# Kernel optimization log

Hardware: AMD Instinct MI355X
Metric: run time of the kernel (lower is better)

## Reference

```python
import jax, jax.numpy as jnp
import numpy as np
from jax import lax

VOCAB = 50257
EMB = 512
HID = 1024
SEQ = 4096
NUM_LAYERS = 2


def _lstm_layer(x_seq, h0, c0, w_ih, w_hh, b_ih, b_hh):
    """Single-layer LSTM over time. x_seq: [T, in], h0/c0: [H].
    PyTorch gate order: i, f, g, o."""
    # Precompute input projections for all timesteps: [T, 4H]
    xg = x_seq @ w_ih.T + (b_ih + b_hh)

    def step(carry, xg_t):
        h, c = carry
        g = xg_t + h @ w_hh.T  # [4H]
        i, f, gg, o = jnp.split(g, 4)
        i = jax.nn.sigmoid(i)
        f = jax.nn.sigmoid(f)
        gg = jnp.tanh(gg)
        o = jax.nn.sigmoid(o)
        c_new = f * c + i * gg
        h_new = o * jnp.tanh(c_new)
        return (h_new, c_new), h_new

    (h_n, c_n), hs = lax.scan(step, (h0, c0), xg)
    return hs, h_n, c_n  # hs: [T, H]


def setup_inputs() -> dict:
    key = jax.random.key(0)
    ks = jax.random.split(key, 12)
    s = 0.02
    inp = {
        "input": jax.random.randint(ks[0], (SEQ,), 0, VOCAB),
        "h0": jnp.zeros((NUM_LAYERS, 1, HID), jnp.float32),
        "c0": jnp.zeros((NUM_LAYERS, 1, HID), jnp.float32),
        "emb": jax.random.normal(ks[1], (VOCAB, EMB), jnp.float32) * s,
        "w_ih0": jax.random.normal(ks[2], (4 * HID, EMB), jnp.float32) * s,
        "w_hh0": jax.random.normal(ks[3], (4 * HID, HID), jnp.float32) * s,
        "b_ih0": jnp.zeros((4 * HID,), jnp.float32),
        "b_hh0": jnp.zeros((4 * HID,), jnp.float32),
        "w_ih1": jax.random.normal(ks[4], (4 * HID, HID), jnp.float32) * s,
        "w_hh1": jax.random.normal(ks[5], (4 * HID, HID), jnp.float32) * s,
        "b_ih1": jnp.zeros((4 * HID,), jnp.float32),
        "b_hh1": jnp.zeros((4 * HID,), jnp.float32),
        "w_out": jax.random.normal(ks[6], (VOCAB, HID), jnp.float32) * s,
        "b_out": jnp.zeros((VOCAB,), jnp.float32),
    }
    return inp


def reference(input, h0, c0, emb, w_ih0, w_hh0, b_ih0, b_hh0,
              w_ih1, w_hh1, b_ih1, b_hh1, w_out, b_out):
    # Embedding gather: [T, EMB] (batch dim of 1 is implicit)
    x = emb[input]
    # Layer 0
    hs0, h_n0, c_n0 = _lstm_layer(x, h0[0, 0], c0[0, 0], w_ih0, w_hh0, b_ih0, b_hh0)
    # Layer 1 consumes layer-0 hidden sequence
    hs1, h_n1, c_n1 = _lstm_layer(hs0, h0[1, 0], c0[1, 0], w_ih1, w_hh1, b_ih1, b_hh1)
    # lstm_out[-1]: [1, H]
    last = hs1[-1][None, :]
    logits = last @ w_out.T + b_out  # [1, VOCAB]
    output = jax.nn.log_softmax(logits, axis=1)
    h_n = jnp.stack([h_n0, h_n1])[:, None, :]  # [2, 1, H]
    c_n = jnp.stack([c_n0, c_n1])[:, None, :]
    return output, h_n, c_n
```

## Files before the change

### kernel.cpp

```cpp
#include <hip/hip_runtime.h>


#define T_SEQ 4096
#define HID   1024
#define EMBD  512
#define VOCAB 50257
#define NBLK  256
#define TPB   256
#define UB    4

#define WS_H0T 0
#define WS_H1T 2048
#define WS_H1F 4096
#define WS_LOG 5120
#define WS_LSE 55377

#define OFF_W0 0
#define OFF_W1 49152
#define OFF_V0 114688
#define OFF_V1 120832
#define OFF_PP 124928
#define OFF_FL 125056
#define SMEM_BYTES 125088

#define FL_SF0 0
#define FL_SF1 1
#define FL_PA1 2
#define FL_C3  3

typedef __attribute__((ext_vector_type(8))) short short8;
typedef __attribute__((ext_vector_type(4))) float f32x4;
typedef unsigned long long u64;

__device__ __forceinline__ unsigned short f2bf(float f) {
  unsigned int u = __float_as_uint(f);
  u += 0x7FFFu + ((u >> 16) & 1u);
  return (unsigned short)(u >> 16);
}
__device__ __forceinline__ unsigned int pack2bf(float a, float b) {
  return (unsigned int)f2bf(a) | ((unsigned int)f2bf(b) << 16);
}
__device__ __forceinline__ float sigmoidf_(float x) {
  return 1.f / (1.f + __expf(-x));
}
__device__ __forceinline__ float tanhf_(float x) {
  return 1.f - 2.f / (__expf(2.f * x) + 1.f);
}
__device__ __forceinline__ unsigned ldsacq(const unsigned* p) {
  return __hip_atomic_load(p, __ATOMIC_ACQUIRE, __HIP_MEMORY_SCOPE_WORKGROUP);
}
__device__ __forceinline__ void ldsrel(unsigned* p, unsigned v) {
  __hip_atomic_store(p, v, __ATOMIC_RELEASE, __HIP_MEMORY_SCOPE_WORKGROUP);
}
__device__ __forceinline__ u64 agld(const u64* p) {
  return __hip_atomic_load(p, __ATOMIC_RELAXED, __HIP_MEMORY_SCOPE_AGENT);
}
__device__ __forceinline__ void agst(u64* p, u64 v) {
  __hip_atomic_store(p, v, __ATOMIC_RELAXED, __HIP_MEMORY_SCOPE_AGENT);
}

template<int NS>
__device__ __forceinline__ f32x4 mm_lds(const short8* vf, const short8* wf,
                                        int grp, int lane) {
  f32x4 a0 = {0.f, 0.f, 0.f, 0.f};
  f32x4 a1 = a0, a2 = a0, a3 = a0;
#pragma unroll
  for (int i = 0; i < NS; ++i) {
    short8 av = vf[i * 4 + grp];
    short8 bv = wf[i * 64 + lane];
    if ((i & 3) == 0)      a0 = __builtin_amdgcn_mfma_f32_16x16x32_bf16(av, bv, a0, 0, 0, 0);
    else if ((i & 3) == 1) a1 = __builtin_amdgcn_mfma_f32_16x16x32_bf16(av, bv, a1, 0, 0, 0);
    else if ((i & 3) == 2) a2 = __builtin_amdgcn_mfma_f32_16x16x32_bf16(av, bv, a2, 0, 0, 0);
    else                   a3 = __builtin_amdgcn_mfma_f32_16x16x32_bf16(av, bv, a3, 0, 0, 0);
  }
  return (a0 + a1) + (a2 + a3);
}

__global__ __launch_bounds__(512, 1) void reset_kernel(
    const float* __restrict__ h0in, unsigned int* __restrict__ ws) {
  const int tid = threadIdx.x;
  u64* H0T = reinterpret_cast<u64*>(ws + WS_H0T);
  u64* H1T = reinterpret_cast<u64*>(ws + WS_H1T);
  agst(&H0T[tid], (u64)pack2bf(h0in[2 * tid], h0in[2 * tid + 1]));
  agst(&H1T[tid], (u64)pack2bf(h0in[HID + 2 * tid], h0in[HID + 2 * tid + 1]));
  agst(&H0T[512 + tid], 0xFFFFFFFF00000000ULL);
  agst(&H1T[512 + tid], 0xFFFFFFFF00000000ULL);
}

__global__ __launch_bounds__(TPB, 1) void scan_kernel(
    const int* __restrict__ tok,
    const float* __restrict__ h0in, const float* __restrict__ c0in,
    const float* __restrict__ emb,
    const float* __restrict__ wih0, const float* __restrict__ whh0,
    const float* __restrict__ bih0, const float* __restrict__ bhh0,
    const float* __restrict__ wih1, const float* __restrict__ whh1,
    const float* __restrict__ bih1, const float* __restrict__ bhh1,
    float* __restrict__ dout, unsigned int* __restrict__ ws) {
  extern __shared__ char smem[];
  short8* W0f = reinterpret_cast<short8*>(smem + OFF_W0);
  short8* W1f = reinterpret_cast<short8*>(smem + OFF_W1);
  unsigned int* v0w = reinterpret_cast<unsigned int*>(smem + OFF_V0);
  unsigned int* v1w = reinterpret_cast<unsigned int*>(smem + OFF_V1);
  const short8* v0f = reinterpret_cast<const short8*>(smem + OFF_V0);
  const short8* v1f = reinterpret_cast<const short8*>(smem + OFF_V1);
  float* pp  = reinterpret_cast<float*>(smem + OFF_PP);
  unsigned* flg = reinterpret_cast<unsigned*>(smem + OFF_FL);

  const int tid = threadIdx.x;
  const int bid = blockIdx.x;
  const int lane = tid & 63;
  const int w = tid >> 6;
  const int grp = lane >> 4;

  for (int slot = tid; slot < 48 * 64; slot += TPB) {
    const int seg = slot >> 6, l = slot & 63;
    const int col = l & 15, g = l >> 4;
    const int grow = (col >> 2) * HID + bid * UB + (col & 3);
    const int k0 = seg * 32 + g * 8;
    const float* src = (k0 < EMBD) ? (wih0 + (size_t)grow * EMBD + k0)
                                   : (whh0 + (size_t)grow * HID + (k0 - EMBD));
    const float4* s4 = reinterpret_cast<const float4*>(src);
    float4 f0 = s4[0], f1 = s4[1];
    short8 pk;
    pk[0] = (short)f2bf(f0.x); pk[1] = (short)f2bf(f0.y);
    pk[2] = (short)f2bf(f0.z); pk[3] = (short)f2bf(f0.w);
    pk[4] = (short)f2bf(f1.x); pk[5] = (short)f2bf(f1.y);
    pk[6] = (short)f2bf(f1.z); pk[7] = (short)f2bf(f1.w);
    W0f[slot] = pk;
  }
  for (int slot = tid; slot < 64 * 64; slot += TPB) {
    const int seg = slot >> 6, l = slot & 63;
    const int col = l & 15, g = l >> 4;
    const int grow = (col >> 2) * HID + bid * UB + (col & 3);
    const int k0 = seg * 32 + g * 8;
    const float* src = (k0 < HID) ? (wih1 + (size_t)grow * HID + k0)
                                  : (whh1 + (size_t)grow * HID + (k0 - HID));
    const float4* s4 = reinterpret_cast<const float4*>(src);
    float4 f0 = s4[0], f1 = s4[1];
    short8 pk;
    pk[0] = (short)f2bf(f0.x); pk[1] = (short)f2bf(f0.y);
    pk[2] = (short)f2bf(f0.z); pk[3] = (short)f2bf(f0.w);
    pk[4] = (short)f2bf(f1.x); pk[5] = (short)f2bf(f1.y);
    pk[6] = (short)f2bf(f1.z); pk[7] = (short)f2bf(f1.w);
    W1f[slot] = pk;
  }
  if (tid < 8) flg[tid] = 1u;

  u64* H0T = reinterpret_cast<u64*>(ws + WS_H0T);
  u64* H1T = reinterpret_cast<u64*>(ws + WS_H1T);

  __syncthreads();

  if (w == 0) {
    float bs0 = 0.f;
    if (lane < 16) {
      const int grow = (lane >> 2) * HID + bid * UB + (lane & 3);
      bs0 = bih0[grow] + bhh0[grow];
    }
    float cst = (lane < UB) ? c0in[bid * UB + lane] : 0.f;

    const float4* e4 = reinterpret_cast<const float4*>(emb) + (size_t)tok[0] * 128;
    float4 xA = e4[lane], xB = e4[64 + lane];

    for (int r = 1; r <= T_SEQ + 1; ++r) {
      const int p = r & 1;
      if (r >= 3) {
        const unsigned need = (unsigned)(r - 2);
        while (ldsacq(&flg[FL_PA1]) < need) { }
      }
      if (r <= T_SEQ) {
        u64* vx = reinterpret_cast<u64*>(v0w + p * 768);
        vx[lane]      = (u64)pack2bf(xA.x, xA.y) | ((u64)pack2bf(xA.z, xA.w) << 32);
        vx[64 + lane] = (u64)pack2bf(xB.x, xB.y) | ((u64)pack2bf(xB.z, xB.w) << 32);
        if (r <= T_SEQ - 1) {
          const float4* en = reinterpret_cast<const float4*>(emb) + (size_t)tok[r] * 128;
          xA = en[lane]; xB = en[64 + lane];
        }
      }
      {
        const unsigned tg = (unsigned)(r - 1);
        const u64* ap = &H0T[((r - 1) & 1) * 512 + lane];
        u64 d0, d1, d2, d3, d4, d5, d6, d7;
        for (;;) {
          d0 = agld(ap);        d1 = agld(ap + 64);  d2 = agld(ap + 128);
          d3 = agld(ap + 192);  d4 = agld(ap + 256); d5 = agld(ap + 320);
          d6 = agld(ap + 384);  d7 = agld(ap + 448);
          if ((unsigned)(d0 >> 32) == tg && (unsigned)(d1 >> 32) == tg &&
              (unsigned)(d2 >> 32) == tg && (unsigned)(d3 >> 32) == tg &&
              (unsigned)(d4 >> 32) == tg && (unsigned)(d5 >> 32) == tg &&
              (unsigned)(d6 >> 32) == tg && (unsigned)(d7 >> 32) == tg) break;
        }
        unsigned* dst = v0w + p * 768 + 256 + lane;
        dst[0] = (unsigned)d0;   dst[64] = (unsigned)d1;
        dst[128] = (unsigned)d2; dst[192] = (unsigned)d3;
        dst[256] = (unsigned)d4; dst[320] = (unsigned)d5;
        dst[384] = (unsigned)d6; dst[448] = (unsigned)d7;
      }
      ldsrel(&flg[FL_SF0], (unsigned)r);

      if (r <= T_SEQ) {
        f32x4 s = mm_lds<48>(v0f + p * 192, W0f, grp, lane);
        float g = (lane < 16) ? (s[0] + bs0) : 0.f;
        const int u = lane & 3;
        const float gi = __shfl(g, u),      gf = __shfl(g, 4 + u);
        const float gg = __shfl(g, 8 + u),  go = __shfl(g, 12 + u);
        float hv = 0.f;
        if (lane < UB) {
          const float c = sigmoidf_(gf) * cst + sigmoidf_(gi) * tanhf_(gg);
          cst = c;
          hv = sigmoidf_(go) * tanhf_(c);
          if (r == T_SEQ) {
            dout[VOCAB + bid * UB + lane] = hv;
            dout[VOCAB + 2 * HID + bid * UB + lane] = c;
          }
        }
        const float a = __shfl(hv, 2 * (lane & 1));
        const float b = __shfl(hv, 2 * (lane & 1) + 1);
        if (lane < 2)
          agst(&H0T[(r & 1) * 512 + bid * 2 + lane],
               ((u64)(unsigned)r << 32) | (u64)pack2bf(a, b));
      }
    }
  } else if (w == 1) {
    for (int r = 2; r <= T_SEQ + 1; ++r) {
      const int p = r & 1;
      if (r >= 4) {
        const unsigned need = (unsigned)(r - 2);
        while (ldsacq(&flg[FL_C3]) < need) { }
      }
      const unsigned tg = (unsigned)(r - 2);
      const u64* ap = &H1T[p * 512 + lane];
      u64 d0, d1, d2, d3, d4, d5, d6, d7;
      for (;;) {
        d0 = agld(ap);        d1 = agld(ap + 64);  d2 = agld(ap + 128);
        d3 = agld(ap + 192);  d4 = agld(ap + 256); d5 = agld(ap + 320);
        d6 = agld(ap + 384);  d7 = agld(ap + 448);
        if ((unsigned)(d0 >> 32) == tg && (unsigned)(d1 >> 32) == tg &&
            (unsigned)(d2 >> 32) == tg && (unsigned)(d3 >> 32) == tg &&
            (unsigned)(d4 >> 32) == tg && (unsigned)(d5 >> 32) == tg &&
            (unsigned)(d6 >> 32) == tg && (unsigned)(d7 >> 32) == tg) break;
      }
      unsigned* dst = v1w + p * 512 + lane;
      dst[0] = (unsigned)d0;   dst[64] = (unsigned)d1;
      dst[128] = (unsigned)d2; dst[192] = (unsigned)d3;
      dst[256] = (unsigned)d4; dst[320] = (unsigned)d5;
      dst[384] = (unsigned)d6; dst[448] = (unsigned)d7;
      ldsrel(&flg[FL_SF1], (unsigned)r);
    }
  } else if (w == 2) {
    for (int r = 2; r <= T_SEQ + 1; ++r) {
      const int p = r & 1;
      const unsigned ru = (unsigned)r;
      while (ldsacq(&flg[FL_SF0]) < ru) { }
      f32x4 s = mm_lds<32>(v0f + p * 192 + 64, W1f, grp, lane);
      if (lane < 16) pp[p * 16 + lane] = s[0];
      ldsrel(&flg[FL_PA1], ru);
    }
  } else {
    float bs1 = 0.f;
    if (lane < 16) {
      const int grow = (lane >> 2) * HID + bid * UB + (lane & 3);
      bs1 = bih1[grow] + bhh1[grow];
    }
    float cst = (lane < UB) ? c0in[HID + bid * UB + lane] : 0.f;
    for (int r = 2; r <= T_SEQ + 1; ++r) {
      const int p = r & 1;
      const unsigned ru = (unsigned)r;
      while (ldsacq(&flg[FL_SF1]) < ru) { }
      f32x4 s = mm_lds<32>(v1f + p * 128, W1f + 32 * 64, grp, lane);
      ldsrel(&flg[FL_C3], ru);
      while (ldsacq(&flg[FL_PA1]) < ru) { }
      float g = (lane < 16) ? (s[0] + pp[p * 16 + lane] + bs1) : 0.f;
      const int u = lane & 3;
      const float gi = __shfl(g, u),      gf = __shfl(g, 4 + u);
      const float gg = __shfl(g, 8 + u),  go = __shfl(g, 12 + u);
      float hv = 0.f;
      if (lane < UB) {
        const float c = sigmoidf_(gf) * cst + sigmoidf_(gi) * tanhf_(gg);
        cst = c;
        hv = sigmoidf_(go) * tanhf_(c);
        if (r == T_SEQ + 1) {
          float* h1f = reinterpret_cast<float*>(ws + WS_H1F);
          h1f[bid * UB + lane] = hv;
          dout[VOCAB + HID + bid * UB + lane] = hv;
          dout[VOCAB + 3 * HID + bid * UB + lane] = c;
        }
      }
      const float a = __shfl(hv, 2 * (lane & 1));
      const float b = __shfl(hv, 2 * (lane & 1) + 1);
      if (lane < 2)
        agst(&H1T[((r - 1) & 1) * 512 + bid * 2 + lane],
             ((u64)(unsigned)(r - 1) << 32) | (u64)pack2bf(a, b));
    }
  }
}

__global__ __launch_bounds__(256) void logits_kernel(
    const float* __restrict__ wout, const float* __restrict__ bout,
    unsigned int* __restrict__ ws) {
  const float* h1f = reinterpret_cast<const float*>(ws + WS_H1F);
  float* lg = reinterpret_cast<float*>(ws + WS_LOG);
  const int lane = threadIdx.x & 63;
  const int wv = threadIdx.x >> 6;
  const int gw = blockIdx.x * 4 + wv;
  const float4* h4 = reinterpret_cast<const float4*>(h1f);
  float4 h[4];
#pragma unroll
  for (int j = 0; j < 4; ++j) h[j] = h4[j * 64 + lane];
  for (int v = gw; v < VOCAB; v += 1024) {
    const float4* wr = reinterpret_cast<const float4*>(wout + (size_t)v * HID);
    float s = 0.f;
#pragma unroll
    for (int j = 0; j < 4; ++j) {
      float4 x = wr[j * 64 + lane];
      s += x.x * h[j].x + x.y * h[j].y + x.z * h[j].z + x.w * h[j].w;
    }
#pragma unroll
    for (int m = 32; m >= 1; m >>= 1) s += __shfl_xor(s, m, 64);
    if (lane == 0) lg[v] = s + bout[v];
  }
}

__global__ __launch_bounds__(1024) void lse_kernel(unsigned int* __restrict__ ws) {
  const float* lg = reinterpret_cast<const float*>(ws + WS_LOG);
  __shared__ float wred[16];
  __shared__ float mshare;
  const int tid = threadIdx.x;
  float m = -3.4e38f;
  for (int i = tid; i < VOCAB; i += 1024) m = fmaxf(m, lg[i]);
#pragma unroll
  for (int s = 32; s >= 1; s >>= 1) m = fmaxf(m, __shfl_xor(m, s, 64));
  if ((tid & 63) == 0) wred[tid >> 6] = m;
  __syncthreads();
  if (tid == 0) {
    float mm = wred[0];
    for (int i = 1; i < 16; ++i) mm = fmaxf(mm, wred[i]);
    mshare = mm;
  }
  __syncthreads();
  const float M = mshare;
  float a = 0.f;
  for (int i = tid; i < VOCAB; i += 1024) a += __expf(lg[i] - M);
#pragma unroll
  for (int s = 32; s >= 1; s >>= 1) a += __shfl_xor(a, s, 64);
  __syncthreads();
  if ((tid & 63) == 0) wred[tid >> 6] = a;
  __syncthreads();
  if (tid == 0) {
    float ss = 0.f;
    for (int i = 0; i < 16; ++i) ss += wred[i];
    reinterpret_cast<float*>(ws + WS_LSE)[0] = M + logf(ss);
  }
}

__global__ __launch_bounds__(256) void out_kernel(
    const unsigned int* __restrict__ ws, float* __restrict__ dout) {
  const float lse = reinterpret_cast<const float*>(ws + WS_LSE)[0];
  const float* lg = reinterpret_cast<const float*>(ws + WS_LOG);
  const int i = blockIdx.x * 256 + threadIdx.x;
  if (i < VOCAB) dout[i] = lg[i] - lse;
}

extern "C" void kernel_launch(void* const* d_in, const int* in_sizes, int n_in,
                              void* d_out, int out_size, void* d_ws, size_t ws_size,
                              hipStream_t stream) {
  const int*   tok  = (const int*)d_in[0];
  const float* h0in = (const float*)d_in[1];
  const float* c0in = (const float*)d_in[2];
  const float* emb  = (const float*)d_in[3];
  const float* wih0 = (const float*)d_in[4];
  const float* whh0 = (const float*)d_in[5];
  const float* bih0 = (const float*)d_in[6];
  const float* bhh0 = (const float*)d_in[7];
  const float* wih1 = (const float*)d_in[8];
  const float* whh1 = (const float*)d_in[9];
  const float* bih1 = (const float*)d_in[10];
  const float* bhh1 = (const float*)d_in[11];
  const float* wout = (const float*)d_in[12];
  const float* bout = (const float*)d_in[13];
  float* out = (float*)d_out;
  unsigned int* ws = (unsigned int*)d_ws;

  (void)in_sizes; (void)n_in; (void)out_size; (void)ws_size;

  (void)hipFuncSetAttribute((const void*)scan_kernel,
                            hipFuncAttributeMaxDynamicSharedMemorySize, SMEM_BYTES);

  reset_kernel<<<1, 512, 0, stream>>>(h0in, ws);
  scan_kernel<<<NBLK, TPB, SMEM_BYTES, stream>>>(
      tok, h0in, c0in, emb, wih0, whh0, bih0, bhh0,
      wih1, whh1, bih1, bhh1, out, ws);
  logits_kernel<<<256, 256, 0, stream>>>(wout, bout, ws);
  lse_kernel<<<1, 1024, 0, stream>>>(ws);
  out_kernel<<<(VOCAB + 255) / 256, 256, 0, stream>>>(ws, out);
}
```

Before: 13.36 ms.

## Mirror hidden-state exchange buffers across eight copies and poll only unready words

```diff
diff --git a/kernel.cpp b/kernel.cpp
--- a/kernel.cpp
+++ b/kernel.cpp
@@ -8,12 +8,13 @@
 #define NBLK  256
 #define TPB   256
 #define UB    4
+#define NMIR  8
 
 #define WS_H0T 0
-#define WS_H1T 2048
-#define WS_H1F 4096
-#define WS_LOG 5120
-#define WS_LSE 55377
+#define WS_H1T 16384
+#define WS_H1F 32768
+#define WS_LOG 33792
+#define WS_LSE 84049
 
 #define OFF_W0 0
 #define OFF_W1 49152
@@ -81,10 +82,15 @@
   const int tid = threadIdx.x;
   u64* H0T = reinterpret_cast<u64*>(ws + WS_H0T);
   u64* H1T = reinterpret_cast<u64*>(ws + WS_H1T);
-  agst(&H0T[tid], (u64)pack2bf(h0in[2 * tid], h0in[2 * tid + 1]));
-  agst(&H1T[tid], (u64)pack2bf(h0in[HID + 2 * tid], h0in[HID + 2 * tid + 1]));
-  agst(&H0T[512 + tid], 0xFFFFFFFF00000000ULL);
-  agst(&H1T[512 + tid], 0xFFFFFFFF00000000ULL);
+  const u64 w0 = (u64)pack2bf(h0in[2 * tid], h0in[2 * tid + 1]);
+  const u64 w1 = (u64)pack2bf(h0in[HID + 2 * tid], h0in[HID + 2 * tid + 1]);
+#pragma unroll
+  for (int m = 0; m < NMIR; ++m) {
+    agst(&H0T[m * 1024 + tid], w0);
+    agst(&H0T[m * 1024 + 512 + tid], 0xFFFFFFFF00000000ULL);
+    agst(&H1T[m * 1024 + tid], w1);
+    agst(&H1T[m * 1024 + 512 + tid], 0xFFFFFFFF00000000ULL);
+  }
 }
 
 __global__ __launch_bounds__(TPB, 1) void scan_kernel(
@@ -111,6 +117,7 @@
   const int lane = tid & 63;
   const int w = tid >> 6;
   const int grp = lane >> 4;
+  const int mymir = bid & 7;
 
   for (int slot = tid; slot < 48 * 64; slot += TPB) {
     const int seg = slot >> 6, l = slot & 63;
@@ -179,16 +186,20 @@
       }
       {
         const unsigned tg = (unsigned)(r - 1);
-        const u64* ap = &H0T[((r - 1) & 1) * 512 + lane];
-        u64 d0, d1, d2, d3, d4, d5, d6, d7;
+        const u64* ap = &H0T[mymir * 1024 + ((r - 1) & 1) * 512 + lane];
+        u64 d0 = 0, d1 = 0, d2 = 0, d3 = 0, d4 = 0, d5 = 0, d6 = 0, d7 = 0;
+        bool k0 = false, k1 = false, k2 = false, k3 = false;
+        bool k4 = false, k5 = false, k6 = false, k7 = false;
         for (;;) {
-          d0 = agld(ap);        d1 = agld(ap + 64);  d2 = agld(ap + 128);
-          d3 = agld(ap + 192);  d4 = agld(ap + 256); d5 = agld(ap + 320);
-          d6 = agld(ap + 384);  d7 = agld(ap + 448);
-          if ((unsigned)(d0 >> 32) == tg && (unsigned)(d1 >> 32) == tg &&
-              (unsigned)(d2 >> 32) == tg && (unsigned)(d3 >> 32) == tg &&
-              (unsigned)(d4 >> 32) == tg && (unsigned)(d5 >> 32) == tg &&
-              (unsigned)(d6 >> 32) == tg && (unsigned)(d7 >> 32) == tg) break;
+          if (!k0) { d0 = agld(ap);       k0 = ((unsigned)(d0 >> 32) == tg); }
+          if (!k1) { d1 = agld(ap + 64);  k1 = ((unsigned)(d1 >> 32) == tg); }
+          if (!k2) { d2 = agld(ap + 128); k2 = ((unsigned)(d2 >> 32) == tg); }
+          if (!k3) { d3 = agld(ap + 192); k3 = ((unsigned)(d3 >> 32) == tg); }
+          if (!k4) { d4 = agld(ap + 256); k4 = ((unsigned)(d4 >> 32) == tg); }
+          if (!k5) { d5 = agld(ap + 320); k5 = ((unsigned)(d5 >> 32) == tg); }
+          if (!k6) { d6 = agld(ap + 384); k6 = ((unsigned)(d6 >> 32) == tg); }
+          if (!k7) { d7 = agld(ap + 448); k7 = ((unsigned)(d7 >> 32) == tg); }
+          if (k0 && k1 && k2 && k3 && k4 && k5 && k6 && k7) break;
         }
         unsigned* dst = v0w + p * 768 + 256 + lane;
         dst[0] = (unsigned)d0;   dst[64] = (unsigned)d1;
@@ -216,8 +227,8 @@
         }
         const float a = __shfl(hv, 2 * (lane & 1));
         const float b = __shfl(hv, 2 * (lane & 1) + 1);
-        if (lane < 2)
-          agst(&H0T[(r & 1) * 512 + bid * 2 + lane],
+        if (lane < 16)
+          agst(&H0T[(lane >> 1) * 1024 + (r & 1) * 512 + bid * 2 + (lane & 1)],
                ((u64)(unsigned)r << 32) | (u64)pack2bf(a, b));
       }
     }
@@ -229,16 +240,20 @@
         while (ldsacq(&flg[FL_C3]) < need) { }
       }
       const unsigned tg = (unsigned)(r - 2);
-      const u64* ap = &H1T[p * 512 + lane];
-      u64 d0, d1, d2, d3, d4, d5, d6, d7;
+      const u64* ap = &H1T[mymir * 1024 + p * 512 + lane];
+      u64 d0 = 0, d1 = 0, d2 = 0, d3 = 0, d4 = 0, d5 = 0, d6 = 0, d7 = 0;
+      bool k0 = false, k1 = false, k2 = false, k3 = false;
+      bool k4 = false, k5 = false, k6 = false, k7 = false;
       for (;;) {
-        d0 = agld(ap);        d1 = agld(ap + 64);  d2 = agld(ap + 128);
-        d3 = agld(ap + 192);  d4 = agld(ap + 256); d5 = agld(ap + 320);
-        d6 = agld(ap + 384);  d7 = agld(ap + 448);
-        if ((unsigned)(d0 >> 32) == tg && (unsigned)(d1 >> 32) == tg &&
-            (unsigned)(d2 >> 32) == tg && (unsigned)(d3 >> 32) == tg &&
-            (unsigned)(d4 >> 32) == tg && (unsigned)(d5 >> 32) == tg &&
-            (unsigned)(d6 >> 32) == tg && (unsigned)(d7 >> 32) == tg) break;
+        if (!k0) { d0 = agld(ap);       k0 = ((unsigned)(d0 >> 32) == tg); }
+        if (!k1) { d1 = agld(ap + 64);  k1 = ((unsigned)(d1 >> 32) == tg); }
+        if (!k2) { d2 = agld(ap + 128); k2 = ((unsigned)(d2 >> 32) == tg); }
+        if (!k3) { d3 = agld(ap + 192); k3 = ((unsigned)(d3 >> 32) == tg); }
+        if (!k4) { d4 = agld(ap + 256); k4 = ((unsigned)(d4 >> 32) == tg); }
+        if (!k5) { d5 = agld(ap + 320); k5 = ((unsigned)(d5 >> 32) == tg); }
+        if (!k6) { d6 = agld(ap + 384); k6 = ((unsigned)(d6 >> 32) == tg); }
+        if (!k7) { d7 = agld(ap + 448); k7 = ((unsigned)(d7 >> 32) == tg); }
+        if (k0 && k1 && k2 && k3 && k4 && k5 && k6 && k7) break;
       }
       unsigned* dst = v1w + p * 512 + lane;
       dst[0] = (unsigned)d0;   dst[64] = (unsigned)d1;
@@ -288,8 +303,8 @@
       }
       const float a = __shfl(hv, 2 * (lane & 1));
       const float b = __shfl(hv, 2 * (lane & 1) + 1);
-      if (lane < 2)
-        agst(&H1T[((r - 1) & 1) * 512 + bid * 2 + lane],
+      if (lane < 16)
+        agst(&H1T[(lane >> 1) * 1024 + ((r - 1) & 1) * 512 + bid * 2 + (lane & 1)],
              ((u64)(unsigned)(r - 1) << 32) | (u64)pack2bf(a, b));
     }
   }
```

Measured after the change: 17.19 ms. +28.7%, slower.

## Split layer-0 recurrent gather across two waves and overlap input MFMAs with polling

Applied to the files above, without the earlier changes.

```diff
diff --git a/kernel.cpp b/kernel.cpp
--- a/kernel.cpp
+++ b/kernel.cpp
@@ -23,10 +23,11 @@
 #define OFF_FL 125056
 #define SMEM_BYTES 125088
 
-#define FL_SF0 0
-#define FL_SF1 1
-#define FL_PA1 2
-#define FL_C3  3
+#define FL_SF0A 0
+#define FL_SF0B 1
+#define FL_SF1  2
+#define FL_PA1  3
+#define FL_C3   4
 
 typedef __attribute__((ext_vector_type(8))) short short8;
 typedef __attribute__((ext_vector_type(4))) float f32x4;
@@ -60,20 +61,14 @@
 }
 
 template<int NS>
-__device__ __forceinline__ f32x4 mm_lds(const short8* vf, const short8* wf,
-                                        int grp, int lane) {
-  f32x4 a0 = {0.f, 0.f, 0.f, 0.f};
-  f32x4 a1 = a0, a2 = a0, a3 = a0;
+__device__ __forceinline__ void mm_acc(f32x4 (&acc)[4], const short8* vf,
+                                       const short8* wf, int grp, int lane) {
 #pragma unroll
   for (int i = 0; i < NS; ++i) {
     short8 av = vf[i * 4 + grp];
     short8 bv = wf[i * 64 + lane];
-    if ((i & 3) == 0)      a0 = __builtin_amdgcn_mfma_f32_16x16x32_bf16(av, bv, a0, 0, 0, 0);
-    else if ((i & 3) == 1) a1 = __builtin_amdgcn_mfma_f32_16x16x32_bf16(av, bv, a1, 0, 0, 0);
-    else if ((i & 3) == 2) a2 = __builtin_amdgcn_mfma_f32_16x16x32_bf16(av, bv, a2, 0, 0, 0);
-    else                   a3 = __builtin_amdgcn_mfma_f32_16x16x32_bf16(av, bv, a3, 0, 0, 0);
-  }
-  return (a0 + a1) + (a2 + a3);
+    acc[i & 3] = __builtin_amdgcn_mfma_f32_16x16x32_bf16(av, bv, acc[i & 3], 0, 0, 0);
+  }
 }
 
 __global__ __launch_bounds__(512, 1) void reset_kernel(
@@ -164,42 +159,52 @@
 
     for (int r = 1; r <= T_SEQ + 1; ++r) {
       const int p = r & 1;
-      if (r >= 3) {
-        const unsigned need = (unsigned)(r - 2);
-        while (ldsacq(&flg[FL_PA1]) < need) { }
-      }
+      f32x4 acc[4];
+      acc[0] = f32x4{0.f, 0.f, 0.f, 0.f};
+      acc[1] = acc[0]; acc[2] = acc[0]; acc[3] = acc[0];
+
       if (r <= T_SEQ) {
         u64* vx = reinterpret_cast<u64*>(v0w + p * 768);
         vx[lane]      = (u64)pack2bf(xA.x, xA.y) | ((u64)pack2bf(xA.z, xA.w) << 32);
         vx[64 + lane] = (u64)pack2bf(xB.x, xB.y) | ((u64)pack2bf(xB.z, xB.w) << 32);
+        mm_acc<16>(acc, v0f + p * 192, W0f, grp, lane);
         if (r <= T_SEQ - 1) {
           const float4* en = reinterpret_cast<const float4*>(emb) + (size_t)tok[r] * 128;
           xA = en[lane]; xB = en[64 + lane];
         }
       }
+
+      if (r >= 3) {
+        const unsigned need = (unsigned)(r - 2);
+        while (ldsacq(&flg[FL_PA1]) < need) { }
+      }
       {
         const unsigned tg = (unsigned)(r - 1);
         const u64* ap = &H0T[((r - 1) & 1) * 512 + lane];
-        u64 d0, d1, d2, d3, d4, d5, d6, d7;
+        u64 d0 = 0, d1 = 0, d2 = 0, d3 = 0;
+        bool k0 = false, k1 = false, k2 = false, k3 = false;
         for (;;) {
-          d0 = agld(ap);        d1 = agld(ap + 64);  d2 = agld(ap + 128);
-          d3 = agld(ap + 192);  d4 = agld(ap + 256); d5 = agld(ap + 320);
-          d6 = agld(ap + 384);  d7 = agld(ap + 448);
-          if ((unsigned)(d0 >> 32) == tg && (unsigned)(d1 >> 32) == tg &&
-              (unsigned)(d2 >> 32) == tg && (unsigned)(d3 >> 32) == tg &&
-              (unsigned)(d4 >> 32) == tg && (unsigned)(d5 >> 32) == tg &&
-              (unsigned)(d6 >> 32) == tg && (unsigned)(d7 >> 32) == tg) break;
+          if (!k0) { d0 = agld(ap);       k0 = ((unsigned)(d0 >> 32) == tg); }
+          if (!k1) { d1 = agld(ap + 64);  k1 = ((unsigned)(d1 >> 32) == tg); }
+          if (!k2) { d2 = agld(ap + 128); k2 = ((unsigned)(d2 >> 32) == tg); }
+          if (!k3) { d3 = agld(ap + 192); k3 = ((unsigned)(d3 >> 32) == tg); }
+          if (k0 && k1 && k2 && k3) break;
         }
         unsigned* dst = v0w + p * 768 + 256 + lane;
         dst[0] = (unsigned)d0;   dst[64] = (unsigned)d1;
         dst[128] = (unsigned)d2; dst[192] = (unsigned)d3;
-        dst[256] = (unsigned)d4; dst[320] = (unsigned)d5;
-        dst[384] = (unsigned)d6; dst[448] = (unsigned)d7;
-      }
-      ldsrel(&flg[FL_SF0], (unsigned)r);
+      }
+      ldsrel(&flg[FL_SF0A], (unsigned)r);
 
       if (r <= T_SEQ) {
-        f32x4 s = mm_lds<48>(v0f + p * 192, W0f, grp, lane);
+        mm_acc<16>(acc, v0f + p * 192 + 64, W0f + 16 * 64, grp, lane);
+        {
+          const unsigned ru = (unsigned)r;
+          while (ldsacq(&flg[FL_SF0B]) < ru) { }
+        }
+        mm_acc<16>(acc, v0f + p * 192 + 128, W0f + 32 * 64, grp, lane);
+
+        f32x4 s = (acc[0] + acc[1]) + (acc[2] + acc[3]);
         float g = (lane < 16) ? (s[0] + bs0) : 0.f;
         const int u = lane & 3;
         const float gi = __shfl(g, u),      gf = __shfl(g, 4 + u);
@@ -209,50 +214,82 @@
           const float c = sigmoidf_(gf) * cst + sigmoidf_(gi) * tanhf_(gg);
           cst = c;
           hv = sigmoidf_(go) * tanhf_(c);
-          if (r == T_SEQ) {
-            dout[VOCAB + bid * UB + lane] = hv;
-            dout[VOCAB + 2 * HID + bid * UB + lane] = c;
-          }
         }
         const float a = __shfl(hv, 2 * (lane & 1));
         const float b = __shfl(hv, 2 * (lane & 1) + 1);
         if (lane < 2)
           agst(&H0T[(r & 1) * 512 + bid * 2 + lane],
                ((u64)(unsigned)r << 32) | (u64)pack2bf(a, b));
+        if (r == T_SEQ && lane < UB) {
+          dout[VOCAB + bid * UB + lane] = hv;
+          dout[VOCAB + 2 * HID + bid * UB + lane] = cst;
+        }
       }
     }
   } else if (w == 1) {
-    for (int r = 2; r <= T_SEQ + 1; ++r) {
+    for (int r = 1; r <= T_SEQ + 1; ++r) {
       const int p = r & 1;
-      if (r >= 4) {
+      if (r >= 3) {
         const unsigned need = (unsigned)(r - 2);
-        while (ldsacq(&flg[FL_C3]) < need) { }
-      }
-      const unsigned tg = (unsigned)(r - 2);
-      const u64* ap = &H1T[p * 512 + lane];
-      u64 d0, d1, d2, d3, d4, d5, d6, d7;
-      for (;;) {
-        d0 = agld(ap);        d1 = agld(ap + 64);  d2 = agld(ap + 128);
-        d3 = agld(ap + 192);  d4 = agld(ap + 256); d5 = agld(ap + 320);
-        d6 = agld(ap + 384);  d7 = agld(ap + 448);
-        if ((unsigned)(d0 >> 32) == tg && (unsigned)(d1 >> 32) == tg &&
-            (unsigned)(d2 >> 32) == tg && (unsigned)(d3 >> 32) == tg &&
-            (unsigned)(d4 >> 32) == tg && (unsigned)(d5 >> 32) == tg &&
-            (unsigned)(d6 >> 32) == tg && (unsigned)(d7 >> 32) == tg) break;
-      }
-      unsigned* dst = v1w + p * 512 + lane;
-      dst[0] = (unsigned)d0;   dst[64] = (unsigned)d1;
-      dst[128] = (unsigned)d2; dst[192] = (unsigned)d3;
-      dst[256] = (unsigned)d4; dst[320] = (unsigned)d5;
-      dst[384] = (unsigned)d6; dst[448] = (unsigned)d7;
-      ldsrel(&flg[FL_SF1], (unsigned)r);
+        while (ldsacq(&flg[FL_PA1]) < need) { }
+      }
+      {
+        const unsigned tg = (unsigned)(r - 1);
+        const u64* ap = &H0T[((r - 1) & 1) * 512 + 256 + lane];
+        u64 d0 = 0, d1 = 0, d2 = 0, d3 = 0;
+        bool k0 = false, k1 = false, k2 = false, k3 = false;
+        for (;;) {
+          if (!k0) { d0 = agld(ap);       k0 = ((unsigned)(d0 >> 32) == tg); }
+          if (!k1) { d1 = agld(ap + 64);  k1 = ((unsigned)(d1 >> 32) == tg); }
+          if (!k2) { d2 = agld(ap + 128); k2 = ((unsigned)(d2 >> 32) == tg); }
+          if (!k3) { d3 = agld(ap + 192); k3 = ((unsigned)(d3 >> 32) == tg); }
+          if (k0 && k1 && k2 && k3) break;
+        }
+        unsigned* dst = v0w + p * 768 + 512 + lane;
+        dst[0] = (unsigned)d0;   dst[64] = (unsigned)d1;
+        dst[128] = (unsigned)d2; dst[192] = (unsigned)d3;
+      }
+      ldsrel(&flg[FL_SF0B], (unsigned)r);
+
+      if (r >= 2) {
+        if (r >= 4) {
+          const unsigned need = (unsigned)(r - 2);
+          while (ldsacq(&flg[FL_C3]) < need) { }
+        }
+        const unsigned tg = (unsigned)(r - 2);
+        const u64* ap = &H1T[p * 512 + lane];
+        u64 d0 = 0, d1 = 0, d2 = 0, d3 = 0, d4 = 0, d5 = 0, d6 = 0, d7 = 0;
+        bool k0 = false, k1 = false, k2 = false, k3 = false;
+        bool k4 = false, k5 = false, k6 = false, k7 = false;
+        for (;;) {
+          if (!k0) { d0 = agld(ap);       k0 = ((unsigned)(d0 >> 32) == tg); }
+          if (!k1) { d1 = agld(ap + 64);  k1 = ((unsigned)(d1 >> 32) == tg); }
+          if (!k2) { d2 = agld(ap + 128); k2 = ((unsigned)(d2 >> 32) == tg); }
+          if (!k3) { d3 = agld(ap + 192); k3 = ((unsigned)(d3 >> 32) == tg); }
+          if (!k4) { d4 = agld(ap + 256); k4 = ((unsigned)(d4 >> 32) == tg); }
+          if (!k5) { d5 = agld(ap + 320); k5 = ((unsigned)(d5 >> 32) == tg); }
+          if (!k6) { d6 = agld(ap + 384); k6 = ((unsigned)(d6 >> 32) == tg); }
+          if (!k7) { d7 = agld(ap + 448); k7 = ((unsigned)(d7 >> 32) == tg); }
+          if (k0 && k1 && k2 && k3 && k4 && k5 && k6 && k7) break;
+        }
+        unsigned* dst = v1w + p * 512 + lane;
+        dst[0] = (unsigned)d0;   dst[64] = (unsigned)d1;
+        dst[128] = (unsigned)d2; dst[192] = (unsigned)d3;
+        dst[256] = (unsigned)d4; dst[320] = (unsigned)d5;
+        dst[384] = (unsigned)d6; dst[448] = (unsigned)d7;
+        ldsrel(&flg[FL_SF1], (unsigned)r);
+      }
     }
   } else if (w == 2) {
     for (int r = 2; r <= T_SEQ + 1; ++r) {
       const int p = r & 1;
       const unsigned ru = (unsigned)r;
-      while (ldsacq(&flg[FL_SF0]) < ru) { }
-      f32x4 s = mm_lds<32>(v0f + p * 192 + 64, W1f, grp, lane);
+      while (ldsacq(&flg[FL_SF0A]) < ru || ldsacq(&flg[FL_SF0B]) < ru) { }
+      f32x4 acc[4];
+      acc[0] = f32x4{0.f, 0.f, 0.f, 0.f};
+      acc[1] = acc[0]; acc[2] = acc[0]; acc[3] = acc[0];
+      mm_acc<32>(acc, v0f + p * 192 + 64, W1f, grp, lane);
+      f32x4 s = (acc[0] + acc[1]) + (acc[2] + acc[3]);
       if (lane < 16) pp[p * 16 + lane] = s[0];
       ldsrel(&flg[FL_PA1], ru);
     }
@@ -267,7 +304,11 @@
       const int p = r & 1;
       const unsigned ru = (unsigned)r;
       while (ldsacq(&flg[FL_SF1]) < ru) { }
-      f32x4 s = mm_lds<32>(v1f + p * 128, W1f + 32 * 64, grp, lane);
+      f32x4 acc[4];
+      acc[0] = f32x4{0.f, 0.f, 0.f, 0.f};
+      acc[1] = acc[0]; acc[2] = acc[0]; acc[3] = acc[0];
+      mm_acc<32>(acc, v1f + p * 128, W1f + 32 * 64, grp, lane);
+      f32x4 s = (acc[0] + acc[1]) + (acc[2] + acc[3]);
       ldsrel(&flg[FL_C3], ru);
       while (ldsacq(&flg[FL_PA1]) < ru) { }
       float g = (lane < 16) ? (s[0] + pp[p * 16 + lane] + bs1) : 0.f;
@@ -283,7 +324,7 @@
           float* h1f = reinterpret_cast<float*>(ws + WS_H1F);
           h1f[bid * UB + lane] = hv;
           dout[VOCAB + HID + bid * UB + lane] = hv;
-          dout[VOCAB + 3 * HID + bid * UB + lane] = c;
+          dout[VOCAB + 3 * HID + bid * UB + lane] = cst;
         }
       }
       const float a = __shfl(hv, 2 * (lane & 1));
```

Result: slower. 15.35 ms (+15.0%).
